# Performance work log

Measured on AMD Instinct MI355X. Metric: run time of the kernel, lower is better.

Reference implementation:

```python
import jax, jax.numpy as jnp
import numpy as np

B, L, NPT, D_TREE = 64, 64, 127, 7  # NPT = 2**D_TREE - 1, heap-layout perfect binary tree
VOCAB, D, LABELS = 30000, 128, 30


def setup_inputs() -> dict:
    key = jax.random.key(0)
    ks = jax.random.split(key, 11)
    s = 0.02
    return {
        "tokens": jax.random.randint(ks[0], (B, L, NPT), 0, VOCAB),
        "mask": jax.random.randint(ks[1], (B, L, L), 0, 2).astype(jnp.int32),
        "emb": jax.random.normal(ks[2], (VOCAB, D), jnp.float32) * s,
        "Wc": jax.random.normal(ks[3], (D, D), jnp.float32) * s,
        "bc": jax.random.normal(ks[4], (D,), jnp.float32) * s,
        "Wq": jax.random.normal(ks[5], (D, D), jnp.float32) * s,
        "Wk": jax.random.normal(ks[6], (D, D), jnp.float32) * s,
        "Wv": jax.random.normal(ks[7], (D, D), jnp.float32) * s,
        "Wo": jax.random.normal(ks[8], (D, D), jnp.float32) * s,
        "Wl": jax.random.normal(ks[9], (D, LABELS), jnp.float32) * s,
        "bl": jax.random.normal(ks[10], (LABELS,), jnp.float32) * s,
    }


def _tree_encode(tokens, emb, Wc, bc):
    # Gather-embed-linear for every node: [B, L, NPT, D]
    e = jnp.einsum("blnd,de->blne", emb[tokens], Wc) + bc
    # Bottom-up subtree sums over heap layout: node k has children 2k+1, 2k+2.
    h = e
    for level in range(D_TREE - 2, -1, -1):
        start, end = 2 ** level - 1, 2 ** (level + 1) - 1
        child = h[:, :, end:end + 2 * (end - start), :]
        child_sum = child[:, :, 0::2, :] + child[:, :, 1::2, :]
        h = h.at[:, :, start:end, :].add(child_sum)
    # max over all subtree-root snapshots and the zero background
    return jnp.maximum(jnp.max(h, axis=2), 0.0)  # [B, L, D]


def reference(tokens, mask, emb, Wc, bc, Wq, Wk, Wv, Wo, Wl, bl):
    enc = _tree_encode(tokens, emb, Wc, bc)  # [B, L, D]
    # masked single-head self-attention (SparseTransformer stand-in)
    q = enc @ Wq
    k = enc @ Wk
    v = enc @ Wv
    scores = jnp.einsum("bqd,bkd->bqk", q, k) / jnp.sqrt(jnp.float32(D))
    scores = jnp.where(mask > 0, scores, jnp.float32(-1e9))
    attn = jax.nn.softmax(scores, axis=-1)
    out = jnp.einsum("bqk,bkd->bqd", attn, v) @ Wo  # [B, L, D]
    pooled = jnp.max(out, axis=1)  # max_pool1d over seq
    return pooled @ Wl + bl  # [B, LABELS]
```

## Files before the change

kernel.cpp:

```cpp
#include <hip/hip_runtime.h>
#include <hip/hip_bf16.h>
#include <math.h>

#define B 64
#define L 64
#define NPT 127
#define D 128
#define VOCAB 30000
#define LABELS 30
#define SPLIT 4
#define KP 132
#define WCS 136

typedef __attribute__((ext_vector_type(8))) short bf16x8;
typedef __attribute__((ext_vector_type(4))) float f32x4;

__device__ __forceinline__ float bfhi(unsigned int u) {
  unsigned int x = u & 0xffff0000u;
  return __builtin_bit_cast(float, x);
}
__device__ __forceinline__ float bflo(unsigned int u) {
  unsigned int x = u << 16;
  return __builtin_bit_cast(float, x);
}
__device__ __forceinline__ unsigned short f2bf(float f) {
  __hip_bfloat16 h = __float2bfloat16(f);
  return __builtin_bit_cast(unsigned short, h);
}

__global__ __launch_bounds__(256) void k0_embWc(const float* __restrict__ emb,
                                                const float* __restrict__ Wc,
                                                const float* __restrict__ bc,
                                                __hip_bfloat16* __restrict__ T) {
  __shared__ unsigned short wcT[D * WCS];
  const int t = threadIdx.x;
  for (int i = t; i < D * D / 4; i += 256) {
    const int d = i >> 5;
    const int e0 = (i & 31) * 4;
    float4 wv = *(const float4*)&Wc[d * D + e0];
    wcT[(e0 + 0) * WCS + d] = f2bf(wv.x);
    wcT[(e0 + 1) * WCS + d] = f2bf(wv.y);
    wcT[(e0 + 2) * WCS + d] = f2bf(wv.z);
    wcT[(e0 + 3) * WCS + d] = f2bf(wv.w);
  }
  __syncthreads();
  const int w = t >> 6, lane = t & 63;
  const int m = lane & 15;
  const int kg = lane >> 4;
  int arow = blockIdx.x * 64 + w * 16 + m;
  if (arow >= VOCAB) arow = VOCAB - 1;
  const float* ap = emb + (size_t)arow * D + kg * 8;
  bf16x8 afrag[4];
#pragma unroll
  for (int kc = 0; kc < 4; ++kc) {
    float4 lo = *(const float4*)(ap + kc * 32);
    float4 hi = *(const float4*)(ap + kc * 32 + 4);
    union { bf16x8 v; unsigned short s[8]; } u;
    u.s[0] = f2bf(lo.x); u.s[1] = f2bf(lo.y); u.s[2] = f2bf(lo.z); u.s[3] = f2bf(lo.w);
    u.s[4] = f2bf(hi.x); u.s[5] = f2bf(hi.y); u.s[6] = f2bf(hi.z); u.s[7] = f2bf(hi.w);
    afrag[kc] = u.v;
  }
  const int grow0 = blockIdx.x * 64 + w * 16 + kg * 4;
#pragma unroll
  for (int ct = 0; ct < 8; ++ct) {
    const int col = ct * 16 + m;
    f32x4 acc = {0.f, 0.f, 0.f, 0.f};
#pragma unroll
    for (int kc = 0; kc < 4; ++kc) {
      bf16x8 bfrag = *(const bf16x8*)&wcT[col * WCS + kc * 32 + kg * 8];
      acc = __builtin_amdgcn_mfma_f32_16x16x32_bf16(afrag[kc], bfrag, acc, 0, 0, 0);
    }
    const float bcv = bc[col];
#pragma unroll
    for (int r = 0; r < 4; ++r) {
      const int grow = grow0 + r;
      if (grow < VOCAB)
        T[(size_t)grow * D + col] = __float2bfloat16(acc[r] + bcv);
    }
  }
}

__global__ __launch_bounds__(512, 4) void k1_tree_qkv(
    const int* __restrict__ tokens, const __hip_bfloat16* __restrict__ T,
    const float* __restrict__ Wq, const float* __restrict__ Wk,
    const float* __restrict__ Wv, float* __restrict__ qb,
    float* __restrict__ kb, float* __restrict__ vb) {
  __shared__ float sEnc[8][D];
  const int t = threadIdx.x;
  const int w = __builtin_amdgcn_readfirstlane(t >> 6);
  const int lane = t & 63;
  const int row = blockIdx.x * 8 + w;
  const int* __restrict__ tokrow = tokens + (size_t)row * NPT;
  const unsigned* Tp = (const unsigned*)T;
  float m0 = -1e30f, m1 = -1e30f;
  float ra0[8], ra1[8];
#pragma unroll
  for (int g = 0; g < 8; ++g) {
    unsigned nl[8], np[4], nq[2], nr;
#pragma unroll
    for (int i = 0; i < 8; ++i)
      nl[i] = Tp[(size_t)tokrow[63 + 8 * g + i] * 64 + lane];
#pragma unroll
    for (int i = 0; i < 4; ++i)
      np[i] = Tp[(size_t)tokrow[31 + 4 * g + i] * 64 + lane];
#pragma unroll
    for (int i = 0; i < 2; ++i)
      nq[i] = Tp[(size_t)tokrow[15 + 2 * g + i] * 64 + lane];
    nr = Tp[(size_t)tokrow[7 + g] * 64 + lane];
    float p0[4], p1[4];
#pragma unroll
    for (int i = 0; i < 4; ++i) {
      float a0 = bflo(nl[2 * i]), a1 = bfhi(nl[2 * i]);
      float b0 = bflo(nl[2 * i + 1]), b1 = bfhi(nl[2 * i + 1]);
      m0 = fmaxf(m0, fmaxf(a0, b0));
      m1 = fmaxf(m1, fmaxf(a1, b1));
      p0[i] = bflo(np[i]) + (a0 + b0);
      p1[i] = bfhi(np[i]) + (a1 + b1);
      m0 = fmaxf(m0, p0[i]);
      m1 = fmaxf(m1, p1[i]);
    }
    float q0[2], q1[2];
#pragma unroll
    for (int i = 0; i < 2; ++i) {
      q0[i] = bflo(nq[i]) + (p0[2 * i] + p0[2 * i + 1]);
      q1[i] = bfhi(nq[i]) + (p1[2 * i] + p1[2 * i + 1]);
      m0 = fmaxf(m0, q0[i]);
      m1 = fmaxf(m1, q1[i]);
    }
    ra0[g] = bflo(nr) + (q0[0] + q0[1]);
    ra1[g] = bfhi(nr) + (q1[0] + q1[1]);
    m0 = fmaxf(m0, ra0[g]);
    m1 = fmaxf(m1, ra1[g]);
  }
  unsigned ns[4], nt0, nt1, n0;
#pragma unroll
  for (int i = 0; i < 4; ++i) ns[i] = Tp[(size_t)tokrow[3 + i] * 64 + lane];
  nt0 = Tp[(size_t)tokrow[1] * 64 + lane];
  nt1 = Tp[(size_t)tokrow[2] * 64 + lane];
  n0 = Tp[(size_t)tokrow[0] * 64 + lane];
  float s0[4], s1[4];
#pragma unroll
  for (int i = 0; i < 4; ++i) {
    s0[i] = bflo(ns[i]) + (ra0[2 * i] + ra0[2 * i + 1]);
    s1[i] = bfhi(ns[i]) + (ra1[2 * i] + ra1[2 * i + 1]);
    m0 = fmaxf(m0, s0[i]);
    m1 = fmaxf(m1, s1[i]);
  }
  float ta0 = bflo(nt0) + (s0[0] + s0[1]);
  float ta1 = bfhi(nt0) + (s1[0] + s1[1]);
  float tb0 = bflo(nt1) + (s0[2] + s0[3]);
  float tb1 = bfhi(nt1) + (s1[2] + s1[3]);
  m0 = fmaxf(m0, fmaxf(ta0, tb0));
  m1 = fmaxf(m1, fmaxf(ta1, tb1));
  float v0 = bflo(n0) + (ta0 + tb0);
  float v1 = bfhi(n0) + (ta1 + tb1);
  m0 = fmaxf(m0, v0);
  m1 = fmaxf(m1, v1);
  sEnc[w][2 * lane] = fmaxf(m0, 0.0f);
  sEnc[w][2 * lane + 1] = fmaxf(m1, 0.0f);
  __syncthreads();
  if (t < 384) {
    const int mi = t >> 7;
    const int c = t & 127;
    const float* W = mi == 0 ? Wq : (mi == 1 ? Wk : Wv);
    float* outb = mi == 0 ? qb : (mi == 1 ? kb : vb);
    float acc[8] = {};
#pragma unroll 8
    for (int k = 0; k < D; ++k) {
      float wv = W[k * D + c];
#pragma unroll
      for (int r = 0; r < 8; ++r) acc[r] += sEnc[r][k] * wv;
    }
    const int row0 = blockIdx.x * 8;
#pragma unroll
    for (int r = 0; r < 8; ++r)
      outb[(size_t)(row0 + r) * D + c] = acc[r];
  }
}

__global__ __launch_bounds__(512) void k2_attn_proj(
    const float* __restrict__ qb, const float* __restrict__ kb,
    const float* __restrict__ vb, const int* __restrict__ mask,
    const float* __restrict__ Wo, float* __restrict__ pool) {
  __shared__ float sK[L * KP];
  __shared__ float sV[L * KP];
  __shared__ float sQ[8][D];
  __shared__ float sOr[16][D];
  __shared__ float pmax[4][D];
  const int t = threadIdx.x;
  const int w = t >> 6, lane = t & 63;
  const int b = blockIdx.x / SPLIT;
  const int sp = blockIdx.x % SPLIT;
  for (int i = t * 4; i < L * D; i += 512 * 4) {
    int r = i >> 7, c = i & 127;
    float4 kv = *(const float4*)&kb[(size_t)(b * L + r) * D + c];
    float4 vv = *(const float4*)&vb[(size_t)(b * L + r) * D + c];
    *(float4*)&sK[r * KP + c] = kv;
    *(float4*)&sV[r * KP + c] = vv;
  }
  __syncthreads();
#pragma unroll
  for (int it = 0; it < 2; ++it) {
    const int r = sp * 16 + w * 2 + it;
    float2 qv = *(const float2*)&qb[(size_t)(b * L + r) * D + lane * 2];
    sQ[w][lane * 2] = qv.x;
    sQ[w][lane * 2 + 1] = qv.y;
    float sc = 0.f;
    const float4* kr = (const float4*)&sK[lane * KP];
    const float4* qr = (const float4*)&sQ[w][0];
#pragma unroll 8
    for (int k4 = 0; k4 < 32; ++k4) {
      float4 kv = kr[k4];
      float4 q4 = qr[k4];
      sc += q4.x * kv.x + q4.y * kv.y + q4.z * kv.z + q4.w * kv.w;
    }
    sc *= 0.08838834764831845f;
    if (mask[((size_t)b * L + r) * L + lane] <= 0) sc = -1e9f;
    float mx = sc;
#pragma unroll
    for (int off = 32; off >= 1; off >>= 1) mx = fmaxf(mx, __shfl_xor(mx, off));
    float ex = __expf(sc - mx);
    float sm = ex;
#pragma unroll
    for (int off = 32; off >= 1; off >>= 1) sm += __shfl_xor(sm, off);
    float a = ex / sm;
    float o0 = 0.f, o1 = 0.f;
#pragma unroll
    for (int j = 0; j < L; ++j) {
      float aj = __shfl(a, j);
      o0 += aj * sV[j * KP + lane];
      o1 += aj * sV[j * KP + lane + 64];
    }
    sOr[w * 2 + it][lane] = o0;
    sOr[w * 2 + it][lane + 64] = o1;
  }
  __syncthreads();
  {
    const int c = t & 127;
    const int rg = t >> 7;
    float acc[4] = {};
#pragma unroll 4
    for (int k = 0; k < D; ++k) {
      float wv = Wo[k * D + c];
#pragma unroll
      for (int r = 0; r < 4; ++r) acc[r] += sOr[rg * 4 + r][k] * wv;
    }
    float pm = fmaxf(fmaxf(acc[0], acc[1]), fmaxf(acc[2], acc[3]));
    pmax[rg][c] = pm;
  }
  __syncthreads();
  if (t < 128) {
    float pv = fmaxf(fmaxf(pmax[0][t], pmax[1][t]), fmaxf(pmax[2][t], pmax[3][t]));
    pool[(size_t)blockIdx.x * D + t] = pv;
  }
}

__global__ __launch_bounds__(128) void k3_logits(const float* __restrict__ pool,
                                                 const float* __restrict__ Wl,
                                                 const float* __restrict__ bl,
                                                 float* __restrict__ out) {
  __shared__ float sP[D];
  const int b = blockIdx.x, t = threadIdx.x;
  float pv = pool[((size_t)b * SPLIT) * D + t];
#pragma unroll
  for (int i = 1; i < SPLIT; ++i)
    pv = fmaxf(pv, pool[((size_t)b * SPLIT + i) * D + t]);
  sP[t] = pv;
  __syncthreads();
  if (t < LABELS) {
    float a = bl[t];
#pragma unroll 4
    for (int d = 0; d < D; ++d) a += sP[d] * Wl[d * LABELS + t];
    out[b * LABELS + t] = a;
  }
}

extern "C" void kernel_launch(void* const* d_in, const int* in_sizes, int n_in,
                              void* d_out, int out_size, void* d_ws, size_t ws_size,
                              hipStream_t stream) {
  const int* tokens = (const int*)d_in[0];
  const int* mask = (const int*)d_in[1];
  const float* emb = (const float*)d_in[2];
  const float* Wc = (const float*)d_in[3];
  const float* bc = (const float*)d_in[4];
  const float* Wq = (const float*)d_in[5];
  const float* Wk = (const float*)d_in[6];
  const float* Wv = (const float*)d_in[7];
  const float* Wo = (const float*)d_in[8];
  const float* Wl = (const float*)d_in[9];
  const float* bl = (const float*)d_in[10];
  float* out = (float*)d_out;

  __hip_bfloat16* T = (__hip_bfloat16*)d_ws;
  float* qb = (float*)(T + (size_t)VOCAB * D);
  float* kb = qb + (size_t)B * L * D;
  float* vb = kb + (size_t)B * L * D;
  float* pool = vb + (size_t)B * L * D;

  hipLaunchKernelGGL(k0_embWc, dim3((VOCAB + 63) / 64), dim3(256), 0, stream,
                     emb, Wc, bc, T);
  hipLaunchKernelGGL(k1_tree_qkv, dim3(B * L / 8), dim3(512), 0, stream,
                     tokens, T, Wq, Wk, Wv, qb, kb, vb);
  hipLaunchKernelGGL(k2_attn_proj, dim3(B * SPLIT), dim3(512), 0, stream,
                     qb, kb, vb, mask, Wo, pool);
  hipLaunchKernelGGL(k3_logits, dim3(B), dim3(128), 0, stream,
                     pool, Wl, bl, out);
}
```

Measured before the change: 75.08 us.

## Split each tree row across two waves with LDS reduction of subtree roots

The k1 tree-encode kernel now uses 1024 threads per block, and two waves share each sequence position. Each wave handles four of the eight depth-3 subtrees and writes the subtree roots and partial maxima to shared memory. After a barrier, one wave finishes the top three levels. The goal is more memory-level parallelism for the gathers, at the cost of an extra barrier, more LDS, and idle waves during the top-level and QKV phases.

```diff
diff --git a/kernel.cpp b/kernel.cpp
--- a/kernel.cpp
+++ b/kernel.cpp
@@ -80,22 +80,28 @@
   }
 }
 
-__global__ __launch_bounds__(512, 4) void k1_tree_qkv(
+__global__ __launch_bounds__(1024, 8) void k1_tree_qkv(
     const int* __restrict__ tokens, const __hip_bfloat16* __restrict__ T,
     const float* __restrict__ Wq, const float* __restrict__ Wk,
     const float* __restrict__ Wv, float* __restrict__ qb,
     float* __restrict__ kb, float* __restrict__ vb) {
+  __shared__ float sR0[8][8][64];
+  __shared__ float sR1[8][8][64];
+  __shared__ float sPM0[8][2][64];
+  __shared__ float sPM1[8][2][64];
   __shared__ float sEnc[8][D];
   const int t = threadIdx.x;
-  const int w = __builtin_amdgcn_readfirstlane(t >> 6);
+  const int wv_ = __builtin_amdgcn_readfirstlane(t >> 6);
   const int lane = t & 63;
-  const int row = blockIdx.x * 8 + w;
+  const int rw = wv_ >> 1;
+  const int half = wv_ & 1;
+  const int row = blockIdx.x * 8 + rw;
   const int* __restrict__ tokrow = tokens + (size_t)row * NPT;
   const unsigned* Tp = (const unsigned*)T;
   float m0 = -1e30f, m1 = -1e30f;
-  float ra0[8], ra1[8];
-#pragma unroll
-  for (int g = 0; g < 8; ++g) {
+#pragma unroll
+  for (int gi = 0; gi < 4; ++gi) {
+    const int g = half * 4 + gi;
     unsigned nl[8], np[4], nq[2], nr;
 #pragma unroll
     for (int i = 0; i < 8; ++i)
@@ -127,37 +133,46 @@
       m0 = fmaxf(m0, q0[i]);
       m1 = fmaxf(m1, q1[i]);
     }
-    ra0[g] = bflo(nr) + (q0[0] + q0[1]);
-    ra1[g] = bfhi(nr) + (q1[0] + q1[1]);
-    m0 = fmaxf(m0, ra0[g]);
-    m1 = fmaxf(m1, ra1[g]);
-  }
-  unsigned ns[4], nt0, nt1, n0;
-#pragma unroll
-  for (int i = 0; i < 4; ++i) ns[i] = Tp[(size_t)tokrow[3 + i] * 64 + lane];
-  nt0 = Tp[(size_t)tokrow[1] * 64 + lane];
-  nt1 = Tp[(size_t)tokrow[2] * 64 + lane];
-  n0 = Tp[(size_t)tokrow[0] * 64 + lane];
-  float s0[4], s1[4];
-#pragma unroll
-  for (int i = 0; i < 4; ++i) {
-    s0[i] = bflo(ns[i]) + (ra0[2 * i] + ra0[2 * i + 1]);
-    s1[i] = bfhi(ns[i]) + (ra1[2 * i] + ra1[2 * i + 1]);
-    m0 = fmaxf(m0, s0[i]);
-    m1 = fmaxf(m1, s1[i]);
-  }
-  float ta0 = bflo(nt0) + (s0[0] + s0[1]);
-  float ta1 = bfhi(nt0) + (s1[0] + s1[1]);
-  float tb0 = bflo(nt1) + (s0[2] + s0[3]);
-  float tb1 = bfhi(nt1) + (s1[2] + s1[3]);
-  m0 = fmaxf(m0, fmaxf(ta0, tb0));
-  m1 = fmaxf(m1, fmaxf(ta1, tb1));
-  float v0 = bflo(n0) + (ta0 + tb0);
-  float v1 = bfhi(n0) + (ta1 + tb1);
-  m0 = fmaxf(m0, v0);
-  m1 = fmaxf(m1, v1);
-  sEnc[w][2 * lane] = fmaxf(m0, 0.0f);
-  sEnc[w][2 * lane + 1] = fmaxf(m1, 0.0f);
+    float r0 = bflo(nr) + (q0[0] + q0[1]);
+    float r1 = bfhi(nr) + (q1[0] + q1[1]);
+    m0 = fmaxf(m0, r0);
+    m1 = fmaxf(m1, r1);
+    sR0[rw][g][lane] = r0;
+    sR1[rw][g][lane] = r1;
+  }
+  sPM0[rw][half][lane] = m0;
+  sPM1[rw][half][lane] = m1;
+  __syncthreads();
+  if (half == 0) {
+    unsigned ns[4], nt0, nt1, n0;
+#pragma unroll
+    for (int i = 0; i < 4; ++i) ns[i] = Tp[(size_t)tokrow[3 + i] * 64 + lane];
+    nt0 = Tp[(size_t)tokrow[1] * 64 + lane];
+    nt1 = Tp[(size_t)tokrow[2] * 64 + lane];
+    n0 = Tp[(size_t)tokrow[0] * 64 + lane];
+    float M0 = fmaxf(sPM0[rw][0][lane], sPM0[rw][1][lane]);
+    float M1 = fmaxf(sPM1[rw][0][lane], sPM1[rw][1][lane]);
+    float s0[4], s1[4];
+#pragma unroll
+    for (int i = 0; i < 4; ++i) {
+      s0[i] = bflo(ns[i]) + (sR0[rw][2 * i][lane] + sR0[rw][2 * i + 1][lane]);
+      s1[i] = bfhi(ns[i]) + (sR1[rw][2 * i][lane] + sR1[rw][2 * i + 1][lane]);
+      M0 = fmaxf(M0, s0[i]);
+      M1 = fmaxf(M1, s1[i]);
+    }
+    float ta0 = bflo(nt0) + (s0[0] + s0[1]);
+    float ta1 = bfhi(nt0) + (s1[0] + s1[1]);
+    float tb0 = bflo(nt1) + (s0[2] + s0[3]);
+    float tb1 = bfhi(nt1) + (s1[2] + s1[3]);
+    M0 = fmaxf(M0, fmaxf(ta0, tb0));
+    M1 = fmaxf(M1, fmaxf(ta1, tb1));
+    float v0 = bflo(n0) + (ta0 + tb0);
+    float v1 = bfhi(n0) + (ta1 + tb1);
+    M0 = fmaxf(M0, v0);
+    M1 = fmaxf(M1, v1);
+    sEnc[rw][2 * lane] = fmaxf(M0, 0.0f);
+    sEnc[rw][2 * lane + 1] = fmaxf(M1, 0.0f);
+  }
   __syncthreads();
   if (t < 384) {
     const int mi = t >> 7;
@@ -167,9 +182,9 @@
     float acc[8] = {};
 #pragma unroll 8
     for (int k = 0; k < D; ++k) {
-      float wv = W[k * D + c];
-#pragma unroll
-      for (int r = 0; r < 8; ++r) acc[r] += sEnc[r][k] * wv;
+      float wvv = W[k * D + c];
+#pragma unroll
+      for (int r = 0; r < 8; ++r) acc[r] += sEnc[r][k] * wvv;
     }
     const int row0 = blockIdx.x * 8;
 #pragma unroll
@@ -299,7 +314,7 @@
 
   hipLaunchKernelGGL(k0_embWc, dim3((VOCAB + 63) / 64), dim3(256), 0, stream,
                      emb, Wc, bc, T);
-  hipLaunchKernelGGL(k1_tree_qkv, dim3(B * L / 8), dim3(512), 0, stream,
+  hipLaunchKernelGGL(k1_tree_qkv, dim3(B * L / 8), dim3(1024), 0, stream,
                      tokens, T, Wq, Wk, Wv, qb, kb, vb);
   hipLaunchKernelGGL(k2_attn_proj, dim3(B * SPLIT), dim3(512), 0, stream,
                      qb, kb, vb, mask, Wo, pool);
```

Measured after the change: 75.08 us. Within noise of the previous version (-0.0%).

## Rewrite attention and output projection with bf16 MFMA tiles

Applied to the files above, without the earlier changes.

The attention kernel now converts K, V (transposed) and Wo (transposed) to bf16 in shared memory and computes QK^T, PV and the Wo projection with 16x16x32 bf16 MFMA instructions instead of scalar FP32 loops. Softmax is reorganised so 32 threads handle each query row, and the probabilities are stored as bf16. This aims to cut ALU work in the attention stage. In exchange it adds bf16 rounding of intermediates and requires each block to transpose and convert Wo on its own.

```diff
diff --git a/kernel.cpp b/kernel.cpp
--- a/kernel.cpp
+++ b/kernel.cpp
@@ -9,8 +9,8 @@
 #define VOCAB 30000
 #define LABELS 30
 #define SPLIT 4
-#define KP 132
 #define WCS 136
+#define VTS 72
 
 typedef __attribute__((ext_vector_type(8))) short bf16x8;
 typedef __attribute__((ext_vector_type(4))) float f32x4;
@@ -167,9 +167,9 @@
     float acc[8] = {};
 #pragma unroll 8
     for (int k = 0; k < D; ++k) {
-      float wv = W[k * D + c];
-#pragma unroll
-      for (int r = 0; r < 8; ++r) acc[r] += sEnc[r][k] * wv;
+      float wvv = W[k * D + c];
+#pragma unroll
+      for (int r = 0; r < 8; ++r) acc[r] += sEnc[r][k] * wvv;
     }
     const int row0 = blockIdx.x * 8;
 #pragma unroll
@@ -182,95 +182,133 @@
     const float* __restrict__ qb, const float* __restrict__ kb,
     const float* __restrict__ vb, const int* __restrict__ mask,
     const float* __restrict__ Wo, float* __restrict__ pool) {
-  __shared__ float sK[L * KP];
-  __shared__ float sV[L * KP];
-  __shared__ float sQ[8][D];
-  __shared__ float sOr[16][D];
-  __shared__ float pmax[4][D];
+  __shared__ unsigned short sK[L * WCS];
+  __shared__ unsigned short sVt[D * VTS];
+  __shared__ unsigned short woT[D * WCS];
+  __shared__ float sS[16 * 68];
+  __shared__ unsigned short sP[16 * VTS];
+  __shared__ unsigned short sO[16 * WCS];
+  __shared__ float pmaxArr[D];
   const int t = threadIdx.x;
-  const int w = t >> 6, lane = t & 63;
+  const int wv_ = t >> 6, lane = t & 63;
+  const int m = lane & 15;
+  const int kg = lane >> 4;
   const int b = blockIdx.x / SPLIT;
   const int sp = blockIdx.x % SPLIT;
   for (int i = t * 4; i < L * D; i += 512 * 4) {
-    int r = i >> 7, c = i & 127;
+    const int r = i >> 7, c = i & 127;
     float4 kv = *(const float4*)&kb[(size_t)(b * L + r) * D + c];
+    ushort4 k4;
+    k4.x = f2bf(kv.x); k4.y = f2bf(kv.y); k4.z = f2bf(kv.z); k4.w = f2bf(kv.w);
+    *(ushort4*)&sK[r * WCS + c] = k4;
     float4 vv = *(const float4*)&vb[(size_t)(b * L + r) * D + c];
-    *(float4*)&sK[r * KP + c] = kv;
-    *(float4*)&sV[r * KP + c] = vv;
-  }
-  __syncthreads();
-#pragma unroll
-  for (int it = 0; it < 2; ++it) {
-    const int r = sp * 16 + w * 2 + it;
-    float2 qv = *(const float2*)&qb[(size_t)(b * L + r) * D + lane * 2];
-    sQ[w][lane * 2] = qv.x;
-    sQ[w][lane * 2 + 1] = qv.y;
-    float sc = 0.f;
-    const float4* kr = (const float4*)&sK[lane * KP];
-    const float4* qr = (const float4*)&sQ[w][0];
-#pragma unroll 8
-    for (int k4 = 0; k4 < 32; ++k4) {
-      float4 kv = kr[k4];
-      float4 q4 = qr[k4];
-      sc += q4.x * kv.x + q4.y * kv.y + q4.z * kv.z + q4.w * kv.w;
-    }
-    sc *= 0.08838834764831845f;
-    if (mask[((size_t)b * L + r) * L + lane] <= 0) sc = -1e9f;
-    float mx = sc;
-#pragma unroll
-    for (int off = 32; off >= 1; off >>= 1) mx = fmaxf(mx, __shfl_xor(mx, off));
-    float ex = __expf(sc - mx);
-    float sm = ex;
-#pragma unroll
-    for (int off = 32; off >= 1; off >>= 1) sm += __shfl_xor(sm, off);
-    float a = ex / sm;
-    float o0 = 0.f, o1 = 0.f;
-#pragma unroll
-    for (int j = 0; j < L; ++j) {
-      float aj = __shfl(a, j);
-      o0 += aj * sV[j * KP + lane];
-      o1 += aj * sV[j * KP + lane + 64];
-    }
-    sOr[w * 2 + it][lane] = o0;
-    sOr[w * 2 + it][lane + 64] = o1;
+    sVt[(c + 0) * VTS + r] = f2bf(vv.x);
+    sVt[(c + 1) * VTS + r] = f2bf(vv.y);
+    sVt[(c + 2) * VTS + r] = f2bf(vv.z);
+    sVt[(c + 3) * VTS + r] = f2bf(vv.w);
+  }
+  for (int i = t; i < D * D / 4; i += 512) {
+    const int d = i >> 5;
+    const int e0 = (i & 31) * 4;
+    float4 wv = *(const float4*)&Wo[d * D + e0];
+    woT[(e0 + 0) * WCS + d] = f2bf(wv.x);
+    woT[(e0 + 1) * WCS + d] = f2bf(wv.y);
+    woT[(e0 + 2) * WCS + d] = f2bf(wv.z);
+    woT[(e0 + 3) * WCS + d] = f2bf(wv.w);
+  }
+  bf16x8 qfrag[4];
+  if (wv_ < 4) {
+    const float* qp = qb + (size_t)(b * L + sp * 16 + m) * D + kg * 8;
+#pragma unroll
+    for (int kc = 0; kc < 4; ++kc) {
+      float4 lo = *(const float4*)(qp + kc * 32);
+      float4 hi = *(const float4*)(qp + kc * 32 + 4);
+      union { bf16x8 v; unsigned short s[8]; } u;
+      u.s[0] = f2bf(lo.x); u.s[1] = f2bf(lo.y); u.s[2] = f2bf(lo.z); u.s[3] = f2bf(lo.w);
+      u.s[4] = f2bf(hi.x); u.s[5] = f2bf(hi.y); u.s[6] = f2bf(hi.z); u.s[7] = f2bf(hi.w);
+      qfrag[kc] = u.v;
+    }
+  }
+  __syncthreads();
+  if (wv_ < 4) {
+    f32x4 acc = {0.f, 0.f, 0.f, 0.f};
+#pragma unroll
+    for (int kc = 0; kc < 4; ++kc) {
+      bf16x8 bfrag = *(const bf16x8*)&sK[(wv_ * 16 + m) * WCS + kc * 32 + kg * 8];
+      acc = __builtin_amdgcn_mfma_f32_16x16x32_bf16(qfrag[kc], bfrag, acc, 0, 0, 0);
+    }
+#pragma unroll
+    for (int r = 0; r < 4; ++r)
+      sS[(kg * 4 + r) * 68 + wv_ * 16 + m] = acc[r];
   }
   __syncthreads();
   {
-    const int c = t & 127;
-    const int rg = t >> 7;
-    float acc[4] = {};
-#pragma unroll 4
-    for (int k = 0; k < D; ++k) {
-      float wv = Wo[k * D + c];
-#pragma unroll
-      for (int r = 0; r < 4; ++r) acc[r] += sOr[rg * 4 + r][k] * wv;
-    }
-    float pm = fmaxf(fmaxf(acc[0], acc[1]), fmaxf(acc[2], acc[3]));
-    pmax[rg][c] = pm;
-  }
-  __syncthreads();
-  if (t < 128) {
-    float pv = fmaxf(fmaxf(pmax[0][t], pmax[1][t]), fmaxf(pmax[2][t], pmax[3][t]));
-    pool[(size_t)blockIdx.x * D + t] = pv;
-  }
+    const int row = t >> 5;
+    const int k2i = (t & 31) * 2;
+    float s0 = sS[row * 68 + k2i] * 0.08838834764831845f;
+    float s1 = sS[row * 68 + k2i + 1] * 0.08838834764831845f;
+    const int* mp = &mask[((size_t)(b * L + sp * 16 + row)) * L + k2i];
+    if (mp[0] <= 0) s0 = -1e9f;
+    if (mp[1] <= 0) s1 = -1e9f;
+    float mx = fmaxf(s0, s1);
+#pragma unroll
+    for (int off = 16; off >= 1; off >>= 1) mx = fmaxf(mx, __shfl_xor(mx, off));
+    float e0 = __expf(s0 - mx), e1 = __expf(s1 - mx);
+    float sm = e0 + e1;
+#pragma unroll
+    for (int off = 16; off >= 1; off >>= 1) sm += __shfl_xor(sm, off);
+    float inv = 1.0f / sm;
+    unsigned short p0 = f2bf(e0 * inv), p1 = f2bf(e1 * inv);
+    *(unsigned*)&sP[row * VTS + k2i] =
+        (unsigned)p0 | ((unsigned)p1 << 16);
+  }
+  __syncthreads();
+  {
+    f32x4 acc = {0.f, 0.f, 0.f, 0.f};
+#pragma unroll
+    for (int kc = 0; kc < 2; ++kc) {
+      bf16x8 pa = *(const bf16x8*)&sP[m * VTS + kc * 32 + kg * 8];
+      bf16x8 vf = *(const bf16x8*)&sVt[(wv_ * 16 + m) * VTS + kc * 32 + kg * 8];
+      acc = __builtin_amdgcn_mfma_f32_16x16x32_bf16(pa, vf, acc, 0, 0, 0);
+    }
+#pragma unroll
+    for (int r = 0; r < 4; ++r)
+      sO[(kg * 4 + r) * WCS + wv_ * 16 + m] = f2bf(acc[r]);
+  }
+  __syncthreads();
+  {
+    f32x4 acc = {0.f, 0.f, 0.f, 0.f};
+#pragma unroll
+    for (int kc = 0; kc < 4; ++kc) {
+      bf16x8 oa = *(const bf16x8*)&sO[m * WCS + kc * 32 + kg * 8];
+      bf16x8 wb = *(const bf16x8*)&woT[(wv_ * 16 + m) * WCS + kc * 32 + kg * 8];
+      acc = __builtin_amdgcn_mfma_f32_16x16x32_bf16(oa, wb, acc, 0, 0, 0);
+    }
+    float v = fmaxf(fmaxf(acc[0], acc[1]), fmaxf(acc[2], acc[3]));
+    v = fmaxf(v, __shfl_xor(v, 16));
+    v = fmaxf(v, __shfl_xor(v, 32));
+    if (kg == 0) pmaxArr[wv_ * 16 + m] = v;
+  }
+  __syncthreads();
+  if (t < D) pool[(size_t)blockIdx.x * D + t] = pmaxArr[t];
 }
 
 __global__ __launch_bounds__(128) void k3_logits(const float* __restrict__ pool,
                                                  const float* __restrict__ Wl,
                                                  const float* __restrict__ bl,
                                                  float* __restrict__ out) {
-  __shared__ float sP[D];
+  __shared__ float sP2[D];
   const int b = blockIdx.x, t = threadIdx.x;
   float pv = pool[((size_t)b * SPLIT) * D + t];
 #pragma unroll
   for (int i = 1; i < SPLIT; ++i)
     pv = fmaxf(pv, pool[((size_t)b * SPLIT + i) * D + t]);
-  sP[t] = pv;
+  sP2[t] = pv;
   __syncthreads();
   if (t < LABELS) {
     float a = bl[t];
 #pragma unroll 4
-    for (int d = 0; d < D; ++d) a += sP[d] * Wl[d * LABELS + t];
+    for (int d = 0; d < D; ++d) a += sP2[d] * Wl[d * LABELS + t];
     out[b * LABELS + t] = a;
   }
 }
```

Result: faster. 64.58 us (-14.0%).
